# Kernel optimization log

Hardware: AMD Instinct MI355X
Metric: run time of the kernel (lower is better)

## Reference

```python
import jax, jax.numpy as jnp
import numpy as np

IN_FEATURES = 4096
OUT_FEATURES = 8192
LUT_SIZE = 65536  # 256 * 256 two-level codebook


def setup_inputs() -> dict:
    key = jax.random.key(0)
    k_x, k_b, k_f, k_s, k_l = jax.random.split(key, 5)
    x = jax.random.normal(k_x, (2, 256, IN_FEATURES), dtype=jnp.float32)
    base_idx = jax.random.randint(k_b, (OUT_FEATURES, IN_FEATURES), 0, 256, dtype=jnp.int32)
    fine_idx = jax.random.randint(k_f, (OUT_FEATURES, IN_FEATURES), 0, 256, dtype=jnp.int32)
    scale = jax.random.uniform(k_s, (OUT_FEATURES, 1), dtype=jnp.float32)
    lut = jax.random.normal(k_l, (LUT_SIZE,), dtype=jnp.float32)
    return {"x": x, "base_idx": base_idx, "fine_idx": fine_idx, "scale": scale, "lut": lut}


def reference(x, base_idx, fine_idx, scale, lut):
    # Two-level LUT dequant: combined 16-bit index = base*256 + fine
    combined_idx = base_idx * 256 + fine_idx              # [out, in] int32
    weights = lut[combined_idx] * scale                   # [out, in] fp32, per-row scale
    # F.linear(x, weights) == x @ weights.T
    return jnp.einsum('bsi,oi->bso', x, weights)
```

## Files before the change

### kernel.cpp

```cpp
#include <hip/hip_runtime.h>

typedef unsigned short ushort_t;
typedef unsigned int   uint32;
typedef __attribute__((ext_vector_type(8)))  short short8;
typedef __attribute__((ext_vector_type(4)))  float floatx4;
typedef __attribute__((ext_vector_type(16))) float floatx16;

#define IN_F   4096
#define OUT_F  8192
#define M_TOT  512

__device__ __forceinline__ ushort_t f2bf(float f) {
    uint32 u = __builtin_bit_cast(uint32, f);
    u += 0x7FFFu + ((u >> 16) & 1u);
    return (ushort_t)(u >> 16);
}
__device__ __forceinline__ uint32 pack2bf(float a, float b) {
    return (uint32)f2bf(a) | ((uint32)f2bf(b) << 16);
}

__global__ void cvt_x_kernel(const float* __restrict__ x, ushort_t* __restrict__ xb) {
    const int g  = blockIdx.x * 256 + threadIdx.x;
    const int r  = g >> 9;
    const int k0 = (g & 511) * 8;
    float4 v0 = *(const float4*)(x + (size_t)r * IN_F + k0);
    float4 v1 = *(const float4*)(x + (size_t)r * IN_F + k0 + 4);
    short8 s;
    s[0] = (short)f2bf(v0.x); s[1] = (short)f2bf(v0.y);
    s[2] = (short)f2bf(v0.z); s[3] = (short)f2bf(v0.w);
    s[4] = (short)f2bf(v1.x); s[5] = (short)f2bf(v1.y);
    s[6] = (short)f2bf(v1.z); s[7] = (short)f2bf(v1.w);
    const int mt = r >> 5;
    const int kt = k0 >> 4;
    ushort_t* dst = xb + ((size_t)(mt * 256 + kt) * 32 + (r & 31)) * 16 + (k0 & 15);
    *(short8*)dst = s;
}

__global__ __launch_bounds__(1024, 4)
void fused_kernel(const ushort_t* __restrict__ xb, const int* __restrict__ base_idx,
                  const int* __restrict__ fine_idx, const float* __restrict__ lut,
                  const float* __restrict__ scale, float* __restrict__ out)
{
    __shared__ ushort_t sh_lut[65536];
    __shared__ ushort_t sh_w[2][32 * 64];

    const int tid  = threadIdx.x;
    const int nblk = blockIdx.x;

    for (int i = tid * 4; i < 65536; i += 4096) {
        float4 v = *(const float4*)(lut + i);
        *(uint32*)&sh_lut[i]     = pack2bf(v.x, v.y);
        *(uint32*)&sh_lut[i + 2] = pack2bf(v.z, v.w);
    }

    const int colr = tid >> 5;
    const int kp   = (tid & 31) * 2;
    const int2* bp = (const int2*)(base_idx + (size_t)(nblk * 32 + colr) * IN_F + kp);
    const int2* fp = (const int2*)(fine_idx + (size_t)(nblk * 32 + colr) * IN_F + kp);
    int2 cb = bp[0],  cf = fp[0];
    int2 nb = bp[32], nf = fp[32];

    const int woff = colr * 64 + ((((kp >> 3) ^ (colr & 7))) << 3) + (kp & 7);

    const int lane = tid & 63;
    const int wave = tid >> 6;
    const int l31  = lane & 31;
    const int lhi  = lane >> 5;

    __syncthreads();

    {
        uint32 w = (uint32)sh_lut[(cb.x << 8) + cf.x]
                 | ((uint32)sh_lut[(cb.y << 8) + cf.y] << 16);
        *(uint32*)&sh_w[0][woff] = w;
    }
    cb = nb; cf = nf;
    nb = bp[64]; nf = fp[64];
    __syncthreads();

    floatx16 acc = {0.f,0.f,0.f,0.f,0.f,0.f,0.f,0.f,0.f,0.f,0.f,0.f,0.f,0.f,0.f,0.f};

    const ushort_t* abase = xb + (size_t)wave * 256 * 512 + l31 * 16 + lhi * 8;
    const int rx8 = (l31 & 7);

#pragma unroll 2
    for (int t = 0; t < 64; ++t) {
        const int cur = t & 1;

        short8 a0 = *(const short8*)(abase + (size_t)(t * 4 + 0) * 512);
        short8 a1 = *(const short8*)(abase + (size_t)(t * 4 + 1) * 512);
        short8 a2 = *(const short8*)(abase + (size_t)(t * 4 + 2) * 512);
        short8 a3 = *(const short8*)(abase + (size_t)(t * 4 + 3) * 512);

        const ushort_t* wb = sh_w[cur];
        short8 b0 = *(const short8*)&wb[l31 * 64 + (((0 + lhi) ^ rx8) << 3)];
        short8 b1 = *(const short8*)&wb[l31 * 64 + (((2 + lhi) ^ rx8) << 3)];
        short8 b2 = *(const short8*)&wb[l31 * 64 + (((4 + lhi) ^ rx8) << 3)];
        short8 b3 = *(const short8*)&wb[l31 * 64 + (((6 + lhi) ^ rx8) << 3)];

        if (t + 1 < 64) {
            uint32 w = (uint32)sh_lut[(cb.x << 8) + cf.x]
                     | ((uint32)sh_lut[(cb.y << 8) + cf.y] << 16);
            *(uint32*)&sh_w[cur ^ 1][woff] = w;
            cb = nb; cf = nf;
            if (t + 3 < 64) { nb = bp[(t + 3) * 32]; nf = fp[(t + 3) * 32]; }
        }

        acc = __builtin_amdgcn_mfma_f32_32x32x16_bf16(a0, b0, acc, 0, 0, 0);
        acc = __builtin_amdgcn_mfma_f32_32x32x16_bf16(a1, b1, acc, 0, 0, 0);
        acc = __builtin_amdgcn_mfma_f32_32x32x16_bf16(a2, b2, acc, 0, 0, 0);
        acc = __builtin_amdgcn_mfma_f32_32x32x16_bf16(a3, b3, acc, 0, 0, 0);

        __syncthreads();
    }

    const float sc = scale[nblk * 32 + l31];
    float* op = out + (size_t)(nblk * 32 + l31);
    const int rbase = wave * 32 + 4 * lhi;
#pragma unroll
    for (int reg = 0; reg < 16; ++reg) {
        const int row = rbase + (reg & 3) + 8 * (reg >> 2);
        op[(size_t)row * OUT_F] = acc[reg] * sc;
    }
}

#define NB  32
#define FBK 128
#define WS  136
#define NITER (IN_F / FBK)
__global__ __launch_bounds__(1024, 4)
void ghost_kernel(const float* __restrict__ xf,
                  const int* __restrict__ base_idx, const int* __restrict__ fine_idx,
                  const float* __restrict__ scale, const float* __restrict__ lut,
                  float* __restrict__ out)
{
    __shared__ ushort_t sh_lut[65536];
    __shared__ ushort_t sh_w[2][NB * WS];
    const int tid = threadIdx.x;
    const int n0  = blockIdx.x * NB;
    for (int i = tid * 4; i < 65536; i += 1024 * 4) {
        float4 v = *(const float4*)(lut + i);
        sh_lut[i + 0] = f2bf(v.x); sh_lut[i + 1] = f2bf(v.y);
        sh_lut[i + 2] = f2bf(v.z); sh_lut[i + 3] = f2bf(v.w);
    }
    const int sn  = tid >> 5;
    const int skq = (tid & 31) * 4;
    const int* bp = base_idx + (size_t)(n0 + sn) * IN_F + skq;
    const int* fp = fine_idx + (size_t)(n0 + sn) * IN_F + skq;
    __syncthreads();
    int4 pb = *(const int4*)(bp);
    int4 pf = *(const int4*)(fp);
    {
        uint32 w0 = (uint32)sh_lut[(pb.x << 8) + pf.x] | ((uint32)sh_lut[(pb.y << 8) + pf.y] << 16);
        uint32 w1 = (uint32)sh_lut[(pb.z << 8) + pf.z] | ((uint32)sh_lut[(pb.w << 8) + pf.w] << 16);
        uint2 wv; wv.x = w0; wv.y = w1;
        *(uint2*)&sh_w[0][sn * WS + skq] = wv;
    }
    pb = *(const int4*)(bp + FBK);
    pf = *(const int4*)(fp + FBK);
    __syncthreads();
    const int lane = tid & 63;
    const int wave = tid >> 6;
    const int l16  = lane & 15;
    const int quad = lane >> 4;
    floatx4 acc[2][2];
    const floatx4 zero = {0.f, 0.f, 0.f, 0.f};
    acc[0][0] = zero; acc[0][1] = zero; acc[1][0] = zero; acc[1][1] = zero;
    const int mrow = wave * 32 + l16;
    const float* xrowf = xf + (size_t)mrow * IN_F + quad * 8;
    for (int t = 0; t < NITER; ++t) {
        const int k0 = t * FBK;
        {
            uint32 w0 = (uint32)sh_lut[(pb.x << 8) + pf.x] | ((uint32)sh_lut[(pb.y << 8) + pf.y] << 16);
            uint32 w1 = (uint32)sh_lut[(pb.z << 8) + pf.z] | ((uint32)sh_lut[(pb.w << 8) + pf.w] << 16);
            uint2 wv; wv.x = w0; wv.y = w1;
            *(uint2*)&sh_w[(t + 1) & 1][sn * WS + skq] = wv;
        }
        {
            const int kk = (t + 2 < NITER ? t + 2 : NITER - 1) * FBK;
            pb = *(const int4*)(bp + kk);
            pf = *(const int4*)(fp + kk);
        }
        const ushort_t* wb = sh_w[t & 1];
#pragma unroll
        for (int ks = 0; ks < 4; ++ks) {
            const int kk = k0 + ks * 32;
            short8 b0 = *(const short8*)&wb[l16        * WS + ks * 32 + quad * 8];
            short8 b1 = *(const short8*)&wb[(16 + l16) * WS + ks * 32 + quad * 8];
            short8 a0, a1;
            const float* p0 = xrowf + kk;
            const float* p1 = xrowf + (size_t)16 * IN_F + kk;
            float4 u0 = *(const float4*)p0, u1 = *(const float4*)(p0 + 4);
            float4 v0 = *(const float4*)p1, v1 = *(const float4*)(p1 + 4);
            a0[0] = (short)f2bf(u0.x); a0[1] = (short)f2bf(u0.y);
            a0[2] = (short)f2bf(u0.z); a0[3] = (short)f2bf(u0.w);
            a0[4] = (short)f2bf(u1.x); a0[5] = (short)f2bf(u1.y);
            a0[6] = (short)f2bf(u1.z); a0[7] = (short)f2bf(u1.w);
            a1[0] = (short)f2bf(v0.x); a1[1] = (short)f2bf(v0.y);
            a1[2] = (short)f2bf(v0.z); a1[3] = (short)f2bf(v0.w);
            a1[4] = (short)f2bf(v1.x); a1[5] = (short)f2bf(v1.y);
            a1[6] = (short)f2bf(v1.z); a1[7] = (short)f2bf(v1.w);
            acc[0][0] = __builtin_amdgcn_mfma_f32_16x16x32_bf16(a0, b0, acc[0][0], 0, 0, 0);
            acc[0][1] = __builtin_amdgcn_mfma_f32_16x16x32_bf16(a0, b1, acc[0][1], 0, 0, 0);
            acc[1][0] = __builtin_amdgcn_mfma_f32_16x16x32_bf16(a1, b0, acc[1][0], 0, 0, 0);
            acc[1][1] = __builtin_amdgcn_mfma_f32_16x16x32_bf16(a1, b1, acc[1][1], 0, 0, 0);
        }
        __syncthreads();
    }
#pragma unroll
    for (int nf = 0; nf < 2; ++nf) {
        const int col = n0 + nf * 16 + l16;
        const float sc = scale[col];
#pragma unroll
        for (int f = 0; f < 2; ++f) {
            const int r0 = wave * 32 + f * 16 + quad * 4;
#pragma unroll
            for (int r = 0; r < 4; ++r) {
                out[(size_t)(r0 + r) * OUT_F + col] = acc[f][nf][r] * sc;
            }
        }
    }
}

extern "C" void kernel_launch(void* const* d_in, const int* in_sizes, int n_in,
                              void* d_out, int out_size, void* d_ws, size_t ws_size,
                              hipStream_t stream) {
    const float* x      = (const float*)d_in[0];
    const int*   bidx   = (const int*)d_in[1];
    const int*   fidx   = (const int*)d_in[2];
    const float* scale  = (const float*)d_in[3];
    const float* lut    = (const float*)d_in[4];
    float*       out    = (float*)d_out;

    const size_t xb_bytes = (size_t)M_TOT * IN_F * sizeof(ushort_t);

    if (ws_size >= xb_bytes) {
        ushort_t* xbuf = (ushort_t*)d_ws;
        cvt_x_kernel<<<1024, 256, 0, stream>>>(x, xbuf);
        fused_kernel<<<256, 1024, 0, stream>>>(xbuf, bidx, fidx, lut, scale, out);
    } else {
        ghost_kernel<<<OUT_F / NB, 1024, 0, stream>>>(x, bidx, fidx, scale, lut, out);
    }
}
```

Baseline: 344.6 us.

## Double the K step per iteration to 128 and use a raw LDS barrier

Each iteration now covers 128 K elements instead of 64. Every thread loads int4 index vectors, does four LUT lookups and writes a uint2 into a doubled, swizzled LDS weight buffer, and the wave issues eight MFMAs per iteration. This halves the number of block-wide barriers and the loop overhead per unit of work. __syncthreads is replaced by an explicit lgkmcnt wait plus s_barrier to avoid waiting on global loads. The costs are more LDS (still within budget), more live registers, and deeper index prefetch.

```diff
diff --git a/kernel.cpp b/kernel.cpp
--- a/kernel.cpp
+++ b/kernel.cpp
@@ -42,7 +42,7 @@
                   const float* __restrict__ scale, float* __restrict__ out)
 {
     __shared__ ushort_t sh_lut[65536];
-    __shared__ ushort_t sh_w[2][32 * 64];
+    __shared__ ushort_t sh_w[2][32 * 128];
 
     const int tid  = threadIdx.x;
     const int nblk = blockIdx.x;
@@ -54,64 +54,91 @@
     }
 
     const int colr = tid >> 5;
-    const int kp   = (tid & 31) * 2;
-    const int2* bp = (const int2*)(base_idx + (size_t)(nblk * 32 + colr) * IN_F + kp);
-    const int2* fp = (const int2*)(fine_idx + (size_t)(nblk * 32 + colr) * IN_F + kp);
-    int2 cb = bp[0],  cf = fp[0];
-    int2 nb = bp[32], nf = fp[32];
-
-    const int woff = colr * 64 + ((((kp >> 3) ^ (colr & 7))) << 3) + (kp & 7);
+    const int kq   = (tid & 31) * 4;
+    const int4* bp = (const int4*)(base_idx + (size_t)(nblk * 32 + colr) * IN_F + kq);
+    const int4* fp = (const int4*)(fine_idx + (size_t)(nblk * 32 + colr) * IN_F + kq);
+
+    const int woff = colr * 128 + (((kq >> 3) ^ (colr & 7)) << 3) + (kq & 7);
 
     const int lane = tid & 63;
     const int wave = tid >> 6;
     const int l31  = lane & 31;
     const int lhi  = lane >> 5;
+    const int rx8  = l31 & 7;
+
+    int4 ib0 = bp[0];
+    int4 if0 = fp[0];
+    int4 Ib  = bp[32];
+    int4 If  = fp[32];
 
     __syncthreads();
 
     {
-        uint32 w = (uint32)sh_lut[(cb.x << 8) + cf.x]
-                 | ((uint32)sh_lut[(cb.y << 8) + cf.y] << 16);
-        *(uint32*)&sh_w[0][woff] = w;
-    }
-    cb = nb; cf = nf;
-    nb = bp[64]; nf = fp[64];
+        uint32 w0 = (uint32)sh_lut[(ib0.x << 8) + if0.x]
+                  | ((uint32)sh_lut[(ib0.y << 8) + if0.y] << 16);
+        uint32 w1 = (uint32)sh_lut[(ib0.z << 8) + if0.z]
+                  | ((uint32)sh_lut[(ib0.w << 8) + if0.w] << 16);
+        uint2 wv; wv.x = w0; wv.y = w1;
+        *(uint2*)&sh_w[0][woff] = wv;
+    }
+    int4 Nb = bp[64];
+    int4 Nf = fp[64];
+
     __syncthreads();
 
     floatx16 acc = {0.f,0.f,0.f,0.f,0.f,0.f,0.f,0.f,0.f,0.f,0.f,0.f,0.f,0.f,0.f,0.f};
 
     const ushort_t* abase = xb + (size_t)wave * 256 * 512 + l31 * 16 + lhi * 8;
-    const int rx8 = (l31 & 7);
 
 #pragma unroll 2
-    for (int t = 0; t < 64; ++t) {
+    for (int t = 0; t < 32; ++t) {
         const int cur = t & 1;
 
-        short8 a0 = *(const short8*)(abase + (size_t)(t * 4 + 0) * 512);
-        short8 a1 = *(const short8*)(abase + (size_t)(t * 4 + 1) * 512);
-        short8 a2 = *(const short8*)(abase + (size_t)(t * 4 + 2) * 512);
-        short8 a3 = *(const short8*)(abase + (size_t)(t * 4 + 3) * 512);
+        short8 a0 = *(const short8*)(abase + (size_t)(t * 8 + 0) * 512);
+        short8 a1 = *(const short8*)(abase + (size_t)(t * 8 + 1) * 512);
+        short8 a2 = *(const short8*)(abase + (size_t)(t * 8 + 2) * 512);
+        short8 a3 = *(const short8*)(abase + (size_t)(t * 8 + 3) * 512);
+        short8 a4 = *(const short8*)(abase + (size_t)(t * 8 + 4) * 512);
+        short8 a5 = *(const short8*)(abase + (size_t)(t * 8 + 5) * 512);
+        short8 a6 = *(const short8*)(abase + (size_t)(t * 8 + 6) * 512);
+        short8 a7 = *(const short8*)(abase + (size_t)(t * 8 + 7) * 512);
 
         const ushort_t* wb = sh_w[cur];
-        short8 b0 = *(const short8*)&wb[l31 * 64 + (((0 + lhi) ^ rx8) << 3)];
-        short8 b1 = *(const short8*)&wb[l31 * 64 + (((2 + lhi) ^ rx8) << 3)];
-        short8 b2 = *(const short8*)&wb[l31 * 64 + (((4 + lhi) ^ rx8) << 3)];
-        short8 b3 = *(const short8*)&wb[l31 * 64 + (((6 + lhi) ^ rx8) << 3)];
-
-        if (t + 1 < 64) {
-            uint32 w = (uint32)sh_lut[(cb.x << 8) + cf.x]
-                     | ((uint32)sh_lut[(cb.y << 8) + cf.y] << 16);
-            *(uint32*)&sh_w[cur ^ 1][woff] = w;
-            cb = nb; cf = nf;
-            if (t + 3 < 64) { nb = bp[(t + 3) * 32]; nf = fp[(t + 3) * 32]; }
+        short8 b0 = *(const short8*)&wb[l31 * 128 + ((( 0 + lhi) ^ rx8) << 3)];
+        short8 b1 = *(const short8*)&wb[l31 * 128 + ((( 2 + lhi) ^ rx8) << 3)];
+        short8 b2 = *(const short8*)&wb[l31 * 128 + ((( 4 + lhi) ^ rx8) << 3)];
+        short8 b3 = *(const short8*)&wb[l31 * 128 + ((( 6 + lhi) ^ rx8) << 3)];
+        short8 b4 = *(const short8*)&wb[l31 * 128 + ((( 8 + lhi) ^ rx8) << 3)];
+        short8 b5 = *(const short8*)&wb[l31 * 128 + (((10 + lhi) ^ rx8) << 3)];
+        short8 b6 = *(const short8*)&wb[l31 * 128 + (((12 + lhi) ^ rx8) << 3)];
+        short8 b7 = *(const short8*)&wb[l31 * 128 + (((14 + lhi) ^ rx8) << 3)];
+
+        if (t < 31) {
+            uint32 w0 = (uint32)sh_lut[(Ib.x << 8) + If.x]
+                      | ((uint32)sh_lut[(Ib.y << 8) + If.y] << 16);
+            uint32 w1 = (uint32)sh_lut[(Ib.z << 8) + If.z]
+                      | ((uint32)sh_lut[(Ib.w << 8) + If.w] << 16);
+            uint2 wv; wv.x = w0; wv.y = w1;
+            *(uint2*)&sh_w[cur ^ 1][woff] = wv;
+            Ib = Nb; If = Nf;
+            if (t + 3 < 32) {
+                Nb = bp[(t + 3) * 32];
+                Nf = fp[(t + 3) * 32];
+            }
         }
 
         acc = __builtin_amdgcn_mfma_f32_32x32x16_bf16(a0, b0, acc, 0, 0, 0);
         acc = __builtin_amdgcn_mfma_f32_32x32x16_bf16(a1, b1, acc, 0, 0, 0);
         acc = __builtin_amdgcn_mfma_f32_32x32x16_bf16(a2, b2, acc, 0, 0, 0);
         acc = __builtin_amdgcn_mfma_f32_32x32x16_bf16(a3, b3, acc, 0, 0, 0);
-
-        __syncthreads();
+        acc = __builtin_amdgcn_mfma_f32_32x32x16_bf16(a4, b4, acc, 0, 0, 0);
+        acc = __builtin_amdgcn_mfma_f32_32x32x16_bf16(a5, b5, acc, 0, 0, 0);
+        acc = __builtin_amdgcn_mfma_f32_32x32x16_bf16(a6, b6, acc, 0, 0, 0);
+        acc = __builtin_amdgcn_mfma_f32_32x32x16_bf16(a7, b7, acc, 0, 0, 0);
+
+        asm volatile("s_waitcnt lgkmcnt(0)" ::: "memory");
+        __builtin_amdgcn_sched_barrier(0);
+        __builtin_amdgcn_s_barrier();
     }
 
     const float sc = scale[nblk * 32 + l31];
```

Result: faster. 326.0 us (-5.4%).
